# Kernel optimization log

Hardware: AMD Instinct MI355X
Metric: run time of the kernel (lower is better)

Reference implementation:

```python
import jax, jax.numpy as jnp
import numpy as np


def setup_inputs() -> dict:
    key = jax.random.key(0)
    ks = jax.random.split(key, 16)
    B, S, D = 2, 2048, 1024
    H, SH, RH = 16, 1, 3
    hd = D // H
    w = 1.0 / np.sqrt(D)
    return {
        "x": jax.random.normal(ks[0], (B, S, D), jnp.float32),
        "Wq": jax.random.normal(ks[1], (D, D), jnp.float32) * w,
        "bq": jnp.zeros((D,), jnp.float32),
        "Wk": jax.random.normal(ks[2], (D, D), jnp.float32) * w,
        "bk": jnp.zeros((D,), jnp.float32),
        "Wv": jax.random.normal(ks[3], (D, D), jnp.float32) * w,
        "bv": jnp.zeros((D,), jnp.float32),
        "Wproj": jax.random.normal(ks[4], (D, D), jnp.float32) * w,
        "bproj": jnp.zeros((D,), jnp.float32),
        "Wr": jax.random.normal(ks[5], (D, H - SH), jnp.float32) * w,
        "br": jnp.zeros((H - SH,), jnp.float32),
        "Ws": jax.random.normal(ks[6], (D, 2), jnp.float32) * w,
        "bs": jnp.zeros((2,), jnp.float32),
        "temperature": jnp.zeros((H, 1, 1), jnp.float32),
        "query_embedding": jax.random.truncated_normal(ks[7], -2.0, 2.0, (H, 1, hd), jnp.float32) * 0.02,
        "num_heads": H,
        "shared_heads": SH,
        "routed_heads": RH,
    }


def reference(x, Wq, bq, Wk, bk, Wv, bv, Wproj, bproj, Wr, br, Ws, bs,
              temperature, query_embedding, num_heads, shared_heads, routed_heads):
    B, S, D = x.shape
    H = num_heads
    hd = D // H

    def split_heads(t):  # [B,S,D] -> [B,H,S,hd]
        return t.reshape(B, S, H, hd).transpose(0, 2, 1, 3)

    q = split_heads(x @ Wq + bq)
    k = split_heads(x @ Wk + bk)
    v = split_heads(x @ Wv + bv)

    # L2-normalize q along head_dim, add learned query embedding, scale by softplus(temperature)
    q_norm = q * jax.lax.rsqrt(jnp.sum(q * q, axis=-1, keepdims=True) + 1e-12)
    q_scaled = (q_norm + query_embedding[None]) * jax.nn.softplus(temperature)[None]

    attn = jnp.einsum('bhqd,bhkd->bhqk', q_scaled, k) / jnp.sqrt(jnp.float32(hd))
    attn = jax.nn.softmax(attn, axis=-1)
    o = jnp.einsum('bhqk,bhkd->bhqd', attn, v)
    o = o.transpose(0, 2, 1, 3).reshape(B, S, D)  # [B,S,D]

    # Routed-head gating via top-k router
    gates = jax.nn.softmax(o @ Wr + br, axis=-1)          # [B,S,H-SH]
    _, idx = jax.lax.top_k(gates, routed_heads)           # [B,S,RH]
    mask = jax.nn.one_hot(idx, H - shared_heads, dtype=gates.dtype).sum(axis=2)
    routed_gates = gates * mask * jnp.float32(routed_heads)

    # Shared-head gating
    sw = jax.nn.softmax(o @ Ws + bs, axis=-1)             # [B,S,2]
    shared_gates = sw * jnp.float32(shared_heads)
    w0 = sw * 2.0
    shared_gates = w0[..., 0:1] * shared_gates
    routed_gates = w0[..., 1:2] * routed_gates
    masked_gates = jnp.concatenate([shared_gates, routed_gates], axis=-1)

    # einsum('bnh,bnd->bnd') sums over h: scales o by sum of gates
    o = masked_gates.sum(axis=-1, keepdims=True) * o
    return o @ Wproj + bproj
```

## Files before the change

kernel.cpp:

```cpp
#include <hip/hip_runtime.h>
#include <hip/hip_bf16.h>

typedef unsigned short ushort_t;
typedef unsigned int uint_t;

typedef __attribute__((ext_vector_type(8))) short bf8;
typedef __attribute__((ext_vector_type(4))) float f4;

__device__ __forceinline__ float bf2f(ushort_t u) {
    unsigned int x = ((unsigned int)u) << 16;
    return __uint_as_float(x);
}
__device__ __forceinline__ ushort_t f2bf(float f) {
    unsigned int x = __float_as_uint(f);
    unsigned int r = x + 0x7fffu + ((x >> 16) & 1u);
    return (ushort_t)(r >> 16);
}
__device__ __forceinline__ uint_t pack2bf(float a, float b) {
    return (uint_t)f2bf(a) | ((uint_t)f2bf(b) << 16);
}

__device__ __forceinline__ void gl2lds16(const ushort_t* g, ushort_t* l) {
    __builtin_amdgcn_global_load_lds(
        (const __attribute__((address_space(1))) void*)g,
        (__attribute__((address_space(3))) void*)l, 16, 0, 0);
}

__global__ __launch_bounds__(256)
void prep(const float* __restrict__ src, ushort_t* __restrict__ dst,
          const float* __restrict__ Wr, const float* __restrict__ Ws,
          ushort_t* __restrict__ Wg)
{
    int bid = blockIdx.x;
    if (bid < 4096) {
        int i = bid * 256 + threadIdx.x;
        float4 v = ((const float4*)src)[i];
        uint2 o;
        o.x = pack2bf(v.x, v.y);
        o.y = pack2bf(v.z, v.w);
        ((uint2*)dst)[i] = o;
    } else {
        int idx = (bid - 4096) * 256 + threadIdx.x;
        int c = idx >> 10, d = idx & 1023;
        float v = 0.f;
        if (c < 15) v = Wr[(size_t)d * 15 + c];
        else if (c < 17) v = Ws[(size_t)d * 2 + (c - 15)];
        Wg[idx] = f2bf(v);
    }
}

__global__ __launch_bounds__(256)
void wtrans(const float* __restrict__ W0, const float* __restrict__ W1,
            const float* __restrict__ W2, const float* __restrict__ W3,
            ushort_t* __restrict__ T0, ushort_t* __restrict__ T1,
            ushort_t* __restrict__ T2, ushort_t* __restrict__ T3)
{
    __shared__ float tile[32][33];
    const float* W; ushort_t* T;
    switch (blockIdx.z) {
        case 0: W = W0; T = T0; break;
        case 1: W = W1; T = T1; break;
        case 2: W = W2; T = T2; break;
        default: W = W3; T = T3; break;
    }
    int k0 = blockIdx.x * 32, n0 = blockIdx.y * 32;
    int t = threadIdx.x;
    int r = t >> 3, c4 = (t & 7) * 4;
    float4 v = *(const float4*)&W[(size_t)(k0 + r) * 1024 + n0 + c4];
    tile[r][c4 + 0] = v.x; tile[r][c4 + 1] = v.y;
    tile[r][c4 + 2] = v.z; tile[r][c4 + 3] = v.w;
    __syncthreads();
    int n = t >> 3, kk = (t & 7) * 4;
    uint2 o;
    o.x = pack2bf(tile[kk][n], tile[kk + 1][n]);
    o.y = pack2bf(tile[kk + 2][n], tile[kk + 3][n]);
    *(uint2*)&T[(size_t)(n0 + n) * 1024 + k0 + kk] = o;
}

__global__ __launch_bounds__(256)
void gemmQKV(const ushort_t* __restrict__ A, const ushort_t* __restrict__ Wt3,
             const float* __restrict__ bq, const float* __restrict__ bk,
             const float* __restrict__ bv,
             ushort_t* __restrict__ Qb, ushort_t* __restrict__ Kw,
             ushort_t* __restrict__ VTw,
             const float* __restrict__ temp, const float* __restrict__ emb)
{
    const int K = 1024;
    __shared__ ushort_t As[128 * 32];
    __shared__ ushort_t Bs[128 * 32];

    int t = threadIdx.x;
    int m0 = blockIdx.x * 128;
    int y = blockIdx.y;
    int region = y >> 3;
    int n0 = (y & 7) * 128;

    int lane = t & 63, w = t >> 6;
    int lm = lane & 15, quad = lane >> 4;
    int wm = (w >> 1) * 64, wn = (w & 1) * 64;

    f4 acc[4][4] = {};

    const ushort_t* pA = &A[(size_t)(m0 + (t >> 2)) * K + (t & 3) * 8];
    const ushort_t* pB = &Wt3[(size_t)(y * 128 + (t >> 2)) * K + (t & 3) * 8];
    ushort_t* lA = &As[t * 8];
    ushort_t* lB = &Bs[t * 8];
    const size_t rstep = (size_t)64 * K;

    for (int k0 = 0; k0 < K; k0 += 32) {
        gl2lds16(pA, lA);
        gl2lds16(pA + rstep, lA + 2048);
        gl2lds16(pB, lB);
        gl2lds16(pB + rstep, lB + 2048);
        pA += 32; pB += 32;
        __syncthreads();

        bf8 af[4], bfr[4];
        #pragma unroll
        for (int mi = 0; mi < 4; mi++)
            af[mi] = *(bf8*)&As[(wm + mi * 16 + lm) * 32 + quad * 8];
        #pragma unroll
        for (int ni = 0; ni < 4; ni++)
            bfr[ni] = *(bf8*)&Bs[(wn + ni * 16 + lm) * 32 + quad * 8];
        if (region == 2) {
            #pragma unroll
            for (int mi = 0; mi < 4; mi++)
            #pragma unroll
            for (int ni = 0; ni < 4; ni++)
                acc[mi][ni] = __builtin_amdgcn_mfma_f32_16x16x32_bf16(af[mi], bfr[ni], acc[mi][ni], 0, 0, 0);
        } else {
            #pragma unroll
            for (int ni = 0; ni < 4; ni++)
            #pragma unroll
            for (int mi = 0; mi < 4; mi++)
                acc[ni][mi] = __builtin_amdgcn_mfma_f32_16x16x32_bf16(bfr[ni], af[mi], acc[ni][mi], 0, 0, 0);
        }
        __syncthreads();
    }

    if (region == 0) {
        int head = (n0 + wn) >> 6;
        float sp = log1pf(__expf(temp[head]));
        f4 bv4[4], ev4[4];
        #pragma unroll
        for (int ni = 0; ni < 4; ni++) {
            bv4[ni] = *(const f4*)&bq[n0 + wn + ni * 16 + quad * 4];
            ev4[ni] = *(const f4*)&emb[head * 64 + ni * 16 + quad * 4];
        }
        #pragma unroll
        for (int mi = 0; mi < 4; mi++) {
            float v[4][4];
            float ss = 0.f;
            #pragma unroll
            for (int ni = 0; ni < 4; ni++)
            #pragma unroll
            for (int i = 0; i < 4; i++) {
                v[ni][i] = acc[ni][mi][i] + bv4[ni][i];
                ss += v[ni][i] * v[ni][i];
            }
            ss += __shfl_xor(ss, 16, 64);
            ss += __shfl_xor(ss, 32, 64);
            float rs = rsqrtf(ss + 1e-12f);
            int tok = m0 + wm + mi * 16 + lm;
            int b = tok >> 11, s = tok & 2047;
            size_t rowb = (((size_t)(b * 16 + head)) * 2048 + s) * 64;
            #pragma unroll
            for (int ni = 0; ni < 4; ni++) {
                uint2 o;
                o.x = pack2bf((v[ni][0] * rs + ev4[ni][0]) * sp * 0.125f,
                              (v[ni][1] * rs + ev4[ni][1]) * sp * 0.125f);
                o.y = pack2bf((v[ni][2] * rs + ev4[ni][2]) * sp * 0.125f,
                              (v[ni][3] * rs + ev4[ni][3]) * sp * 0.125f);
                *(uint2*)&Qb[rowb + ni * 16 + quad * 4] = o;
            }
        }
    } else if (region == 1) {
        int head = (n0 + wn) >> 6;
        f4 bv4[4];
        #pragma unroll
        for (int ni = 0; ni < 4; ni++)
            bv4[ni] = *(const f4*)&bk[n0 + wn + ni * 16 + quad * 4];
        #pragma unroll
        for (int mi = 0; mi < 4; mi++) {
            int tok = m0 + wm + mi * 16 + lm;
            int b = tok >> 11, s = tok & 2047;
            size_t rowb = (((size_t)(b * 16 + head)) * 2048 + s) * 64;
            #pragma unroll
            for (int ni = 0; ni < 4; ni++) {
                uint2 o;
                o.x = pack2bf(acc[ni][mi][0] + bv4[ni][0], acc[ni][mi][1] + bv4[ni][1]);
                o.y = pack2bf(acc[ni][mi][2] + bv4[ni][2], acc[ni][mi][3] + bv4[ni][3]);
                *(uint2*)&Kw[rowb + ni * 16 + quad * 4] = o;
            }
        }
    } else {
        float bvv[4];
        #pragma unroll
        for (int ni = 0; ni < 4; ni++) bvv[ni] = bv[n0 + wn + ni * 16 + lm];
        #pragma unroll
        for (int mi = 0; mi < 4; mi++) {
            int gr0 = m0 + wm + mi * 16 + quad * 4;
            int b = gr0 >> 11, s0 = gr0 & 2047;
            #pragma unroll
            for (int ni = 0; ni < 4; ni++) {
                int gc = n0 + wn + ni * 16 + lm;
                int h = gc >> 6, d = gc & 63;
                uint2 o;
                o.x = pack2bf(acc[mi][ni][0] + bvv[ni], acc[mi][ni][1] + bvv[ni]);
                o.y = pack2bf(acc[mi][ni][2] + bvv[ni], acc[mi][ni][3] + bvv[ni]);
                *(uint2*)&VTw[(((size_t)(b * 16 + h)) * 64 + d) * 2048 + s0] = o;
            }
        }
    }
}

__global__ __launch_bounds__(256)
void gemmP(const ushort_t* __restrict__ A, const ushort_t* __restrict__ Wt,
           const float* __restrict__ bias, const float* __restrict__ G,
           float* __restrict__ out, int M, int N, int K)
{
    __shared__ ushort_t As[128 * 32];
    __shared__ ushort_t Bs[128 * 32];

    int t = threadIdx.x;
    int m0 = blockIdx.x * 128, n0 = blockIdx.y * 128;
    int lane = t & 63, w = t >> 6;
    int lm = lane & 15, quad = lane >> 4;
    int wm = (w >> 1) * 64, wn = (w & 1) * 64;

    f4 acc[4][4] = {};

    const ushort_t* pA = &A[(size_t)(m0 + (t >> 2)) * K + (t & 3) * 8];
    const ushort_t* pB = &Wt[(size_t)(n0 + (t >> 2)) * K + (t & 3) * 8];
    ushort_t* lA = &As[t * 8];
    ushort_t* lB = &Bs[t * 8];
    const size_t rstep = (size_t)64 * K;

    for (int k0 = 0; k0 < K; k0 += 32) {
        gl2lds16(pA, lA);
        gl2lds16(pA + rstep, lA + 2048);
        gl2lds16(pB, lB);
        gl2lds16(pB + rstep, lB + 2048);
        pA += 32; pB += 32;
        __syncthreads();

        bf8 af[4], bfr[4];
        #pragma unroll
        for (int mi = 0; mi < 4; mi++)
            af[mi] = *(bf8*)&As[(wm + mi * 16 + lm) * 32 + quad * 8];
        #pragma unroll
        for (int ni = 0; ni < 4; ni++)
            bfr[ni] = *(bf8*)&Bs[(wn + ni * 16 + lm) * 32 + quad * 8];
        #pragma unroll
        for (int ni = 0; ni < 4; ni++)
        #pragma unroll
        for (int mi = 0; mi < 4; mi++)
            acc[ni][mi] = __builtin_amdgcn_mfma_f32_16x16x32_bf16(bfr[ni], af[mi], acc[ni][mi], 0, 0, 0);
        __syncthreads();
    }

    f4 bv4[4];
    #pragma unroll
    for (int ni = 0; ni < 4; ni++)
        bv4[ni] = *(const f4*)&bias[n0 + wn + ni * 16 + quad * 4];
    #pragma unroll
    for (int mi = 0; mi < 4; mi++) {
        int tok = m0 + wm + mi * 16 + lm;
        float g = G[tok];
        size_t rowb = (size_t)tok * N + n0 + wn;
        #pragma unroll
        for (int ni = 0; ni < 4; ni++) {
            f4 o;
            #pragma unroll
            for (int i = 0; i < 4; i++) o[i] = g * acc[ni][mi][i] + bv4[ni][i];
            *(f4*)&out[rowb + ni * 16 + quad * 4] = o;
        }
    }
}

__global__ __launch_bounds__(256)
void attn(const ushort_t* __restrict__ Q, const ushort_t* __restrict__ K,
          const ushort_t* __restrict__ VT, ushort_t* __restrict__ O)
{
    __shared__ ushort_t Ks[64 * 72];
    __shared__ ushort_t Vt[64 * 72];
    __shared__ ushort_t Ps[4][16 * 72];

    int t = threadIdx.x, lane = t & 63, w = t >> 6;
    int lm = lane & 15, quad = lane >> 4;
    int bid = blockIdx.x;
    int bh = bid & 31, qt = bid >> 5;
    size_t base = (size_t)bh * 2048 * 64;

    const ushort_t* qp = &Q[base + (size_t)(qt * 64 + w * 16 + lm) * 64 + quad * 8];
    bf8 qa0 = *(const bf8*)qp;
    bf8 qa1 = *(const bf8*)(qp + 32);

    float l_part = 0.f;
    f4 o_acc[4] = {};

    int sr = t >> 3, sc = (t & 7) * 8;
    const ushort_t* kg0 = &K[base + (size_t)sr * 64 + sc];
    const ushort_t* vg0 = &VT[base + (size_t)sr * 2048 + sc];

    for (int kb = 0; kb < 2048; kb += 64) {
        __syncthreads();
        {
            uint4 k0 = *(const uint4*)(kg0 + (size_t)kb * 64);
            uint4 k1 = *(const uint4*)(kg0 + (size_t)(kb + 32) * 64);
            uint4 v0 = *(const uint4*)(vg0 + kb);
            uint4 v1 = *(const uint4*)(vg0 + 32 * 2048 + kb);
            *(uint4*)&Ks[sr * 72 + sc] = k0;
            *(uint4*)&Ks[(sr + 32) * 72 + sc] = k1;
            *(uint4*)&Vt[sr * 72 + sc] = v0;
            *(uint4*)&Vt[(sr + 32) * 72 + sc] = v1;
        }
        __syncthreads();

        f4 s_acc[4] = {};
        #pragma unroll
        for (int kt = 0; kt < 4; kt++) {
            bf8 k0 = *(bf8*)&Ks[(kt * 16 + lm) * 72 + quad * 8];
            bf8 k1 = *(bf8*)&Ks[(kt * 16 + lm) * 72 + 32 + quad * 8];
            s_acc[kt] = __builtin_amdgcn_mfma_f32_16x16x32_bf16(k0, qa0, s_acc[kt], 0, 0, 0);
            s_acc[kt] = __builtin_amdgcn_mfma_f32_16x16x32_bf16(k1, qa1, s_acc[kt], 0, 0, 0);
        }

        ushort_t* pw = &Ps[w][0];
        #pragma unroll
        for (int kt = 0; kt < 4; kt++) {
            float p0 = __expf(s_acc[kt][0]);
            float p1 = __expf(s_acc[kt][1]);
            float p2 = __expf(s_acc[kt][2]);
            float p3 = __expf(s_acc[kt][3]);
            l_part += (p0 + p1) + (p2 + p3);
            *(uint_t*)&pw[lm * 72 + kt * 16 + quad * 4] = pack2bf(p0, p1);
            *(uint_t*)&pw[lm * 72 + kt * 16 + quad * 4 + 2] = pack2bf(p2, p3);
        }

        bf8 pb0 = *(bf8*)&pw[lm * 72 + quad * 8];
        bf8 pb1 = *(bf8*)&pw[lm * 72 + 32 + quad * 8];
        #pragma unroll
        for (int dt = 0; dt < 4; dt++) {
            bf8 v0 = *(bf8*)&Vt[(dt * 16 + lm) * 72 + quad * 8];
            bf8 v1 = *(bf8*)&Vt[(dt * 16 + lm) * 72 + 32 + quad * 8];
            o_acc[dt] = __builtin_amdgcn_mfma_f32_16x16x32_bf16(v0, pb0, o_acc[dt], 0, 0, 0);
            o_acc[dt] = __builtin_amdgcn_mfma_f32_16x16x32_bf16(v1, pb1, o_acc[dt], 0, 0, 0);
        }
    }

    l_part += __shfl_xor(l_part, 16, 64);
    l_part += __shfl_xor(l_part, 32, 64);
    float rl = 1.f / l_part;

    int b = bh >> 4, h = bh & 15;
    int tok = qt * 64 + w * 16 + lm;
    size_t rowb = ((size_t)(b * 2048 + tok)) * 1024 + h * 64;
    #pragma unroll
    for (int dt = 0; dt < 4; dt++) {
        uint2 o;
        o.x = pack2bf(o_acc[dt][0] * rl, o_acc[dt][1] * rl);
        o.y = pack2bf(o_acc[dt][2] * rl, o_acc[dt][3] * rl);
        *(uint2*)&O[rowb + dt * 16 + quad * 4] = o;
    }
}

__global__ __launch_bounds__(256)
void router(const ushort_t* __restrict__ O, const ushort_t* __restrict__ Wg,
            const float* __restrict__ br, const float* __restrict__ bs,
            float* __restrict__ G)
{
    __shared__ float Ls[64][21];
    int t = threadIdx.x, lane = t & 63, w = t >> 6;
    int lm = lane & 15, quad = lane >> 4;
    int tok0 = blockIdx.x * 64;

    const ushort_t* ap = &O[(size_t)(tok0 + w * 16 + lm) * 1024 + quad * 8];
    const ushort_t* b0p = &Wg[(size_t)lm * 1024 + quad * 8];
    const ushort_t* b1p = &Wg[(size_t)(16 + lm) * 1024 + quad * 8];

    f4 acc0 = {}, acc1 = {};
    for (int k0 = 0; k0 < 1024; k0 += 32) {
        bf8 a = *(const bf8*)(ap + k0);
        bf8 b0 = *(const bf8*)(b0p + k0);
        bf8 b1 = *(const bf8*)(b1p + k0);
        acc0 = __builtin_amdgcn_mfma_f32_16x16x32_bf16(a, b0, acc0, 0, 0, 0);
        acc1 = __builtin_amdgcn_mfma_f32_16x16x32_bf16(a, b1, acc1, 0, 0, 0);
    }
    #pragma unroll
    for (int i = 0; i < 4; i++) {
        int tl = w * 16 + quad * 4 + i;
        Ls[tl][lm] = acc0[i];
        if (lm == 0) Ls[tl][16] = acc1[i];
    }
    __syncthreads();
    if (t < 64) {
        float v[15];
        float mx = -1e30f;
        #pragma unroll
        for (int c = 0; c < 15; c++) { v[c] = Ls[t][c] + br[c]; mx = fmaxf(mx, v[c]); }
        float sum = 0.f;
        #pragma unroll
        for (int c = 0; c < 15; c++) { v[c] = __expf(v[c] - mx); sum += v[c]; }
        float inv = 1.f / sum;
        float t3 = 0.f;
        for (int r = 0; r < 3; r++) {
            int bi = 0; float bv = -1e30f;
            #pragma unroll
            for (int c = 0; c < 15; c++) if (v[c] > bv) { bv = v[c]; bi = c; }
            t3 += bv; v[bi] = -1e30f;
        }
        t3 *= inv;
        float a0 = Ls[t][15] + bs[0], a1 = Ls[t][16] + bs[1];
        float m2 = fmaxf(a0, a1);
        float e0 = __expf(a0 - m2), e1 = __expf(a1 - m2);
        G[tok0 + t] = (2.f * e0 + 6.f * e1 * t3) / (e0 + e1);
    }
}

extern "C" void kernel_launch(void* const* d_in, const int* in_sizes, int n_in,
                              void* d_out, int out_size, void* d_ws, size_t ws_size,
                              hipStream_t stream)
{
    const float* x     = (const float*)d_in[0];
    const float* Wq    = (const float*)d_in[1];
    const float* bq    = (const float*)d_in[2];
    const float* Wk    = (const float*)d_in[3];
    const float* bk    = (const float*)d_in[4];
    const float* Wv    = (const float*)d_in[5];
    const float* bv    = (const float*)d_in[6];
    const float* Wproj = (const float*)d_in[7];
    const float* bproj = (const float*)d_in[8];
    const float* Wr    = (const float*)d_in[9];
    const float* br    = (const float*)d_in[10];
    const float* Ws    = (const float*)d_in[11];
    const float* bs    = (const float*)d_in[12];
    const float* temp  = (const float*)d_in[13];
    const float* emb   = (const float*)d_in[14];

    const int M = 4096, N = 1024, Kd = 1024;

    char* ws = (char*)d_ws;
    ushort_t* Kw  = (ushort_t*)ws;
    ushort_t* VTw = (ushort_t*)(ws + 8388608);
    ushort_t* Qb  = (ushort_t*)(ws + 16777216);
    ushort_t* Ob  = (ushort_t*)(ws + 25165824);
    ushort_t* xb  = (ushort_t*)(ws + 33554432);
    ushort_t* Wt3 = (ushort_t*)(ws + 41943040);
    ushort_t* Wtp = (ushort_t*)(ws + 48234496);
    float*    Gw  = (float*)(ws + 50331648);
    ushort_t* Wg  = (ushort_t*)(ws + 50348032);

    prep<<<4224, 256, 0, stream>>>(x, xb, Wr, Ws, Wg);
    wtrans<<<dim3(32, 32, 4), 256, 0, stream>>>(Wq, Wk, Wv, Wproj,
        Wt3, Wt3 + 1048576, Wt3 + 2097152, Wtp);

    gemmQKV<<<dim3(32, 24), 256, 0, stream>>>(xb, Wt3, bq, bk, bv,
        Qb, Kw, VTw, temp, emb);

    attn<<<1024, 256, 0, stream>>>(Qb, Kw, VTw, Ob);

    router<<<64, 256, 0, stream>>>(Ob, Wg, br, bs, Gw);

    gemmP<<<dim3(32, 8), 256, 0, stream>>>(Ob, Wtp, bproj, Gw, (float*)d_out, M, N, Kd);
}
```

Measured before the change: 271.3 us.

## Use 32x32x16 MFMA tiles with 128 queries per attention block

The attention kernel moves from 16x16x32 to 32x32x16 bf16 MFMA instructions. Each wave now handles 32 query rows, so a block covers 128 queries and the grid halves to 512 blocks. Every K/V tile loaded into LDS is therefore reused across twice as many queries, which cuts global and LDS traffic per FLOP. In exchange, the larger accumulators raise register pressure, the P scratch buffer in LDS doubles, and fewer blocks means less parallelism across CUs.

```diff
diff --git a/kernel.cpp b/kernel.cpp
--- a/kernel.cpp
+++ b/kernel.cpp
@@ -6,6 +6,7 @@
 
 typedef __attribute__((ext_vector_type(8))) short bf8;
 typedef __attribute__((ext_vector_type(4))) float f4;
+typedef __attribute__((ext_vector_type(16))) float f16v;
 
 __device__ __forceinline__ float bf2f(ushort_t u) {
     unsigned int x = ((unsigned int)u) << 16;
@@ -284,20 +285,22 @@
 {
     __shared__ ushort_t Ks[64 * 72];
     __shared__ ushort_t Vt[64 * 72];
-    __shared__ ushort_t Ps[4][16 * 72];
+    __shared__ ushort_t Ps[4][32 * 72];
 
     int t = threadIdx.x, lane = t & 63, w = t >> 6;
-    int lm = lane & 15, quad = lane >> 4;
+    int l31 = lane & 31, hi = lane >> 5;
     int bid = blockIdx.x;
     int bh = bid & 31, qt = bid >> 5;
     size_t base = (size_t)bh * 2048 * 64;
 
-    const ushort_t* qp = &Q[base + (size_t)(qt * 64 + w * 16 + lm) * 64 + quad * 8];
-    bf8 qa0 = *(const bf8*)qp;
-    bf8 qa1 = *(const bf8*)(qp + 32);
+    int tok = qt * 128 + w * 32 + l31;
+    const ushort_t* qp = &Q[base + (size_t)tok * 64 + hi * 8];
+    bf8 qa[4];
+    #pragma unroll
+    for (int c = 0; c < 4; c++) qa[c] = *(const bf8*)(qp + c * 16);
 
     float l_part = 0.f;
-    f4 o_acc[4] = {};
+    f16v o_acc[2] = {};
 
     int sr = t >> 3, sc = (t & 7) * 8;
     const ushort_t* kg0 = &K[base + (size_t)sr * 64 + sc];
@@ -317,51 +320,53 @@
         }
         __syncthreads();
 
-        f4 s_acc[4] = {};
-        #pragma unroll
-        for (int kt = 0; kt < 4; kt++) {
-            bf8 k0 = *(bf8*)&Ks[(kt * 16 + lm) * 72 + quad * 8];
-            bf8 k1 = *(bf8*)&Ks[(kt * 16 + lm) * 72 + 32 + quad * 8];
-            s_acc[kt] = __builtin_amdgcn_mfma_f32_16x16x32_bf16(k0, qa0, s_acc[kt], 0, 0, 0);
-            s_acc[kt] = __builtin_amdgcn_mfma_f32_16x16x32_bf16(k1, qa1, s_acc[kt], 0, 0, 0);
-        }
-
         ushort_t* pw = &Ps[w][0];
         #pragma unroll
-        for (int kt = 0; kt < 4; kt++) {
-            float p0 = __expf(s_acc[kt][0]);
-            float p1 = __expf(s_acc[kt][1]);
-            float p2 = __expf(s_acc[kt][2]);
-            float p3 = __expf(s_acc[kt][3]);
-            l_part += (p0 + p1) + (p2 + p3);
-            *(uint_t*)&pw[lm * 72 + kt * 16 + quad * 4] = pack2bf(p0, p1);
-            *(uint_t*)&pw[lm * 72 + kt * 16 + quad * 4 + 2] = pack2bf(p2, p3);
-        }
-
-        bf8 pb0 = *(bf8*)&pw[lm * 72 + quad * 8];
-        bf8 pb1 = *(bf8*)&pw[lm * 72 + 32 + quad * 8];
-        #pragma unroll
-        for (int dt = 0; dt < 4; dt++) {
-            bf8 v0 = *(bf8*)&Vt[(dt * 16 + lm) * 72 + quad * 8];
-            bf8 v1 = *(bf8*)&Vt[(dt * 16 + lm) * 72 + 32 + quad * 8];
-            o_acc[dt] = __builtin_amdgcn_mfma_f32_16x16x32_bf16(v0, pb0, o_acc[dt], 0, 0, 0);
-            o_acc[dt] = __builtin_amdgcn_mfma_f32_16x16x32_bf16(v1, pb1, o_acc[dt], 0, 0, 0);
-        }
-    }
-
-    l_part += __shfl_xor(l_part, 16, 64);
+        for (int kt2 = 0; kt2 < 2; kt2++) {
+            f16v s = {};
+            #pragma unroll
+            for (int c = 0; c < 4; c++) {
+                bf8 kf = *(bf8*)&Ks[(kt2 * 32 + l31) * 72 + c * 16 + hi * 8];
+                s = __builtin_amdgcn_mfma_f32_32x32x16_bf16(kf, qa[c], s, 0, 0, 0);
+            }
+            #pragma unroll
+            for (int g = 0; g < 4; g++) {
+                float p0 = __expf(s[g * 4 + 0]);
+                float p1 = __expf(s[g * 4 + 1]);
+                float p2 = __expf(s[g * 4 + 2]);
+                float p3 = __expf(s[g * 4 + 3]);
+                l_part += (p0 + p1) + (p2 + p3);
+                int k0i = kt2 * 32 + g * 8 + hi * 4;
+                *(uint_t*)&pw[l31 * 72 + k0i]     = pack2bf(p0, p1);
+                *(uint_t*)&pw[l31 * 72 + k0i + 2] = pack2bf(p2, p3);
+            }
+        }
+
+        #pragma unroll
+        for (int c = 0; c < 4; c++) {
+            bf8 pf = *(bf8*)&pw[l31 * 72 + c * 16 + hi * 8];
+            #pragma unroll
+            for (int dt = 0; dt < 2; dt++) {
+                bf8 vf = *(bf8*)&Vt[(dt * 32 + l31) * 72 + c * 16 + hi * 8];
+                o_acc[dt] = __builtin_amdgcn_mfma_f32_32x32x16_bf16(vf, pf, o_acc[dt], 0, 0, 0);
+            }
+        }
+    }
+
     l_part += __shfl_xor(l_part, 32, 64);
     float rl = 1.f / l_part;
 
     int b = bh >> 4, h = bh & 15;
-    int tok = qt * 64 + w * 16 + lm;
     size_t rowb = ((size_t)(b * 2048 + tok)) * 1024 + h * 64;
     #pragma unroll
-    for (int dt = 0; dt < 4; dt++) {
+    for (int dt = 0; dt < 2; dt++)
+    #pragma unroll
+    for (int g = 0; g < 4; g++) {
+        int d0 = dt * 32 + g * 8 + hi * 4;
         uint2 o;
-        o.x = pack2bf(o_acc[dt][0] * rl, o_acc[dt][1] * rl);
-        o.y = pack2bf(o_acc[dt][2] * rl, o_acc[dt][3] * rl);
-        *(uint2*)&O[rowb + dt * 16 + quad * 4] = o;
+        o.x = pack2bf(o_acc[dt][g * 4 + 0] * rl, o_acc[dt][g * 4 + 1] * rl);
+        o.y = pack2bf(o_acc[dt][g * 4 + 2] * rl, o_acc[dt][g * 4 + 3] * rl);
+        *(uint2*)&O[rowb + d0] = o;
     }
 }
 
@@ -458,7 +463,7 @@
     gemmQKV<<<dim3(32, 24), 256, 0, stream>>>(xb, Wt3, bq, bk, bv,
         Qb, Kw, VTw, temp, emb);
 
-    attn<<<1024, 256, 0, stream>>>(Qb, Kw, VTw, Ob);
+    attn<<<512, 256, 0, stream>>>(Qb, Kw, VTw, Ob);
 
     router<<<64, 256, 0, stream>>>(Ob, Wg, br, bs, Gw);
 
```

Result: faster. 263.7 us (-2.8%).
